# Kernel tuning notes

Hardware: AMD Instinct MI355X
Metric: run time of the kernel (lower is better)

## Reference

```python
import jax, jax.numpy as jnp
import numpy as np

DIM_MODEL = 1024
DIM_K = 1024
DIM_V = 1024


def setup_inputs() -> dict:
    key = jax.random.key(0)
    ks = jax.random.split(key, 7)
    B, S = 4, 2048
    scale = 1.0 / np.sqrt(DIM_MODEL)
    return {
        "x": jax.random.normal(ks[0], (B, S, DIM_MODEL), dtype=jnp.float32),
        # weights stored [in, out] (transpose of torch Linear.weight)
        "Wq": jax.random.normal(ks[1], (DIM_MODEL, DIM_K), dtype=jnp.float32) * scale,
        "Wk": jax.random.normal(ks[2], (DIM_MODEL, DIM_K), dtype=jnp.float32) * scale,
        "Wv": jax.random.normal(ks[3], (DIM_MODEL, DIM_V), dtype=jnp.float32) * scale,
        "Wo": jax.random.normal(ks[4], (DIM_V, DIM_MODEL), dtype=jnp.float32) * (1.0 / np.sqrt(DIM_V)),
        "ln2_gamma": jnp.ones((DIM_MODEL,), dtype=jnp.float32),
        "ln2_beta": jnp.zeros((DIM_MODEL,), dtype=jnp.float32),
    }


def _layernorm(x, gamma, beta, eps=1e-5):
    mu = jnp.mean(x, axis=-1, keepdims=True)
    var = jnp.var(x, axis=-1, keepdims=True)
    return (x - mu) * jax.lax.rsqrt(var + eps) * gamma + beta


def reference(x, Wq, Wk, Wv, Wo, ln2_gamma, ln2_beta):
    # single-head attention, x: [B,S,D]
    q = jnp.einsum("bsd,dk->bsk", x, Wq)
    k = jnp.einsum("bsd,dk->bsk", x, Wk)
    v = jnp.einsum("bsd,dv->bsv", x, Wv)
    scores = jnp.einsum("bqk,bsk->bqs", q, k) / jnp.sqrt(jnp.asarray(DIM_K, x.dtype))
    attn = jax.nn.softmax(scores, axis=-1)  # [B,S,S]
    ctx = jnp.einsum("bqs,bsv->bqv", attn, v)
    hidden = jnp.einsum("bqv,vd->bqd", ctx, Wo)
    hidden = _layernorm(hidden, ln2_gamma, ln2_beta)
    return hidden
```

## Files before the change

kernel.cpp:

```cpp
#include <hip/hip_runtime.h>
#include <hip/hip_bf16.h>
#include <stdint.h>

typedef __bf16 bf16;
typedef __attribute__((ext_vector_type(8))) __bf16 bf16x8;
typedef __attribute__((ext_vector_type(4))) __bf16 bf16x4;
typedef __attribute__((ext_vector_type(4))) float f32x4;

#define AS1 __attribute__((address_space(1)))
#define AS3 __attribute__((address_space(3)))

__device__ __forceinline__ void gl_lds16(const void* g, void* l) {
  __builtin_amdgcn_global_load_lds((const AS1 uint32_t*)g, (AS3 uint32_t*)l, 16, 0, 0);
}

#define FENCE() asm volatile("" ::: "memory")
#define BAR()                        \
  do {                               \
    FENCE();                         \
    __builtin_amdgcn_s_barrier();    \
    FENCE();                         \
  } while (0)
#define VMW4() asm volatile("s_waitcnt vmcnt(4)" ::: "memory")

template <int MODE>
__global__ __launch_bounds__(512, 2) void gemm256(
    const bf16* __restrict__ Abase, const bf16* __restrict__ Bbase,
    bf16* __restrict__ Cbase, int K, int lda, int ldb, int ldc,
    long long sA, long long sB, long long sC, float alpha,
    float* __restrict__ lsum, bf16* __restrict__ C2, bf16* __restrict__ C3) {
  extern __shared__ char smem[];
  const int z = blockIdx.z;
  const bf16* A = Abase + (long long)z * sA;
  const bf16* B = Bbase + (long long)z * sB;
  bf16* C = Cbase + (long long)z * sC;
  const int m0 = blockIdx.y * 256, n0 = blockIdx.x * 256;
  const int t = threadIdx.x;
  const int lane = t & 63;
  const int wid = t >> 6, wrow = wid >> 2, wcol = wid & 3;
  const int quad = lane >> 4, r = lane & 15;

  const int rowq = t >> 3;
  const int chunk = (t & 7) ^ (rowq & 7);
  const bf16* pA0 = A + (long long)(m0 + rowq) * lda + chunk * 8;
  const bf16* pB0 = B + (long long)(n0 + rowq) * ldb + chunk * 8;

  const int aoff = (wrow * 64 + r) * 128;
  const int boff = 32768 + (wcol * 32 + r) * 128;
  const int cs0 = ((quad) ^ (r & 7)) * 16;
  const int cs1 = ((4 + quad) ^ (r & 7)) * 16;

#define STAGE_A(HALF, KT, SB)                                                  \
  do {                                                                         \
    gl_lds16(pA0 + (long long)((HALF) * 128) * lda + (KT),                     \
             (SB) + (HALF) * 16384 + t * 16);                                  \
    gl_lds16(pA0 + (long long)((HALF) * 128 + 64) * lda + (KT),                \
             (SB) + (HALF) * 16384 + 8192 + t * 16);                           \
  } while (0)
#define STAGE_B(HALF, KT, SB)                                                  \
  do {                                                                         \
    gl_lds16(pB0 + (long long)((HALF) * 128) * ldb + (KT),                     \
             (SB) + 32768 + (HALF) * 16384 + t * 16);                          \
    gl_lds16(pB0 + (long long)((HALF) * 128 + 64) * ldb + (KT),                \
             (SB) + 32768 + (HALF) * 16384 + 8192 + t * 16);                   \
  } while (0)
#define READ_A(MH)                                                             \
  _Pragma("unroll") for (int mr = 0; mr < 4; ++mr) {                           \
    af[mr][0] = *(const bf16x8*)(Sc + (MH) * 16384 + aoff + mr * 2048 + cs0);  \
    af[mr][1] = *(const bf16x8*)(Sc + (MH) * 16384 + aoff + mr * 2048 + cs1);  \
  }
#define READ_B(NH)                                                             \
  _Pragma("unroll") for (int nr = 0; nr < 2; ++nr) {                           \
    bfr[NH][nr][0] =                                                           \
        *(const bf16x8*)(Sc + (NH) * 16384 + boff + nr * 2048 + cs0);          \
    bfr[NH][nr][1] =                                                           \
        *(const bf16x8*)(Sc + (NH) * 16384 + boff + nr * 2048 + cs1);          \
  }
#define MMA(MH, NH)                                                            \
  _Pragma("unroll") for (int mr = 0; mr < 4; ++mr)                             \
      _Pragma("unroll") for (int nr = 0; nr < 2; ++nr) {                       \
    acc[MH][NH][mr][nr] = __builtin_amdgcn_mfma_f32_16x16x32_bf16(             \
        af[mr][0], bfr[NH][nr][0], acc[MH][NH][mr][nr], 0, 0, 0);              \
    acc[MH][NH][mr][nr] = __builtin_amdgcn_mfma_f32_16x16x32_bf16(             \
        af[mr][1], bfr[NH][nr][1], acc[MH][NH][mr][nr], 0, 0, 0);              \
  }

  f32x4 acc[2][2][4][2] = {};
  bf16x8 af[4][2];
  bf16x8 bfr[2][2][2];
  char* Sc = smem;
  char* Sn = smem + 65536;
  const int T = K >> 6;

  STAGE_A(0, 0, Sc);
  STAGE_B(0, 0, Sc);
  STAGE_A(1, 0, Sc);
  STAGE_B(1, 0, Sc);
  {
    const int kt1p = (T > 1) ? 64 : 0;
    STAGE_A(0, kt1p, Sn);
    STAGE_B(0, kt1p, Sn);
  }
  VMW4();
  BAR();

  for (int tt = 0; tt < T; ++tt) {
    const int kt1 = (tt + 1 < T ? tt + 1 : 0) << 6;
    const int kt2 = (tt + 2 < T ? tt + 2 : 0) << 6;
    READ_A(0);
    READ_B(0);
    STAGE_A(1, kt1, Sn);
    __builtin_amdgcn_s_setprio(1);
    MMA(0, 0);
    __builtin_amdgcn_s_setprio(0);
    BAR();
    READ_B(1);
    STAGE_B(1, kt1, Sn);
    __builtin_amdgcn_s_setprio(1);
    MMA(0, 1);
    __builtin_amdgcn_s_setprio(0);
    BAR();
    READ_A(1);
    STAGE_A(0, kt2, Sc);
    __builtin_amdgcn_s_setprio(1);
    MMA(1, 0);
    __builtin_amdgcn_s_setprio(0);
    BAR();
    STAGE_B(0, kt2, Sc);
    __builtin_amdgcn_s_setprio(1);
    MMA(1, 1);
    __builtin_amdgcn_s_setprio(0);
    VMW4();
    BAR();
    char* tp = Sc;
    Sc = Sn;
    Sn = tp;
  }

#pragma unroll
  for (int mh = 0; mh < 2; ++mh)
#pragma unroll
    for (int mr = 0; mr < 4; ++mr) {
      const int row0 = m0 + mh * 128 + wrow * 64 + mr * 16 + quad * 4;
      float rsum[4] = {0.f, 0.f, 0.f, 0.f};
#pragma unroll
      for (int nh = 0; nh < 2; ++nh)
#pragma unroll
        for (int nr = 0; nr < 2; ++nr) {
          const int col = n0 + nh * 128 + wcol * 32 + nr * 16 + r;
#pragma unroll
          for (int rg = 0; rg < 4; ++rg) {
            float v = acc[mh][nh][mr][nr][rg] * alpha;
            if constexpr (MODE == 1) {
              bf16 eb = (bf16)__expf(v);
              C[(long long)(row0 + rg) * ldc + col] = eb;
              rsum[rg] += (float)eb;
            } else {
              C[(long long)(row0 + rg) * ldc + col] = (bf16)v;
            }
          }
        }
      if constexpr (MODE == 1) {
#pragma unroll
        for (int rg = 0; rg < 4; ++rg) {
#pragma unroll
          for (int off = 8; off >= 1; off >>= 1)
            rsum[rg] += __shfl_xor(rsum[rg], off);
          if (r == 0)
            atomicAdd(&lsum[(long long)z * 2048 + row0 + rg], rsum[rg]);
        }
      }
    }
#undef STAGE_A
#undef STAGE_B
#undef READ_A
#undef READ_B
#undef MMA
}

template <int MODE>
__global__ __launch_bounds__(256, 3) void gemm128(
    const bf16* __restrict__ Abase, const bf16* __restrict__ Bbase,
    bf16* __restrict__ Cbase, int K, int lda, int ldb, int ldc,
    long long sA, long long sB, long long sC, float alpha,
    float* __restrict__ lsum, bf16* __restrict__ C2, bf16* __restrict__ C3,
    const bf16* __restrict__ A2) {
  extern __shared__ char smem[];
  const int z = blockIdx.z;
  const int bx = blockIdx.x, by = blockIdx.y;
  const bf16* A;
  const bf16* B;
  int m0, n0;
  bool urole = false;
  if constexpr (MODE == 4) {
    if (bx >= 16) {
      urole = true;
      A = A2;
      B = Abase;
      m0 = (bx - 16) * 128;
      n0 = by * 128;
    } else {
      A = Abase;
      B = Bbase;
      m0 = by * 128;
      n0 = bx * 128;
    }
  } else {
    A = Abase + (long long)z * sA;
    B = Bbase + (long long)z * sB;
    m0 = by * 128;
    n0 = bx * 128;
  }
  bf16* C = Cbase + (long long)z * sC;
  const int t = threadIdx.x;
  const int lane = t & 63, wave = t >> 6;
  const int wm = (wave >> 1) * 64, wn = (wave & 1) * 64;
  const int quad = lane >> 4, r = lane & 15;

  const int srow = t >> 3;
  const int schunk = (t & 7) ^ (srow & 7);
  const bf16* ga = A + (long long)(m0 + srow) * lda + schunk * 8;
  const bf16* gb = B + (long long)(n0 + srow) * ldb + schunk * 8;
  if constexpr (MODE == 5) {
    ga += (long long)z * K;
    gb += (long long)z * K;
  }
  char* la = smem + t * 16;
  char* lb = smem + 16384 + t * 16;

  f32x4 acc[4][4] = {};

  for (int k0 = 0; k0 < K; k0 += 64) {
    __syncthreads();
#pragma unroll
    for (int rd = 0; rd < 4; rd++) {
      gl_lds16(ga + (long long)(32 * rd) * lda, la + rd * 4096);
      gl_lds16(gb + (long long)(32 * rd) * ldb, lb + rd * 4096);
    }
    ga += 64;
    gb += 64;
    __syncthreads();

#pragma unroll
    for (int kk = 0; kk < 2; kk++) {
      bf16x8 af[4], bfr[4];
      const int csa = ((kk * 4 + quad) ^ (r & 7)) * 16;
      const char* pa = smem + (wm + r) * 128 + csa;
      const char* pb = smem + 16384 + (wn + r) * 128 + csa;
#pragma unroll
      for (int i = 0; i < 4; i++) af[i] = *(const bf16x8*)(pa + i * 2048);
#pragma unroll
      for (int j = 0; j < 4; j++) bfr[j] = *(const bf16x8*)(pb + j * 2048);
#pragma unroll
      for (int i = 0; i < 4; i++)
#pragma unroll
        for (int j = 0; j < 4; j++)
          acc[i][j] = __builtin_amdgcn_mfma_f32_16x16x32_bf16(af[i], bfr[j],
                                                              acc[i][j], 0, 0, 0);
    }
  }

  if constexpr (MODE == 5) {
    float* Cf = ((float*)Cbase) + (long long)z * 1024 * 1024;
#pragma unroll
    for (int i = 0; i < 4; i++) {
      const int row0 = m0 + wm + i * 16 + quad * 4;
#pragma unroll
      for (int j = 0; j < 4; j++) {
        const int col = n0 + wn + j * 16 + r;
#pragma unroll
        for (int rg = 0; rg < 4; rg++)
          Cf[(long long)(row0 + rg) * 1024 + col] = acc[i][j][rg];
      }
    }
    return;
  }
  if constexpr (MODE == 4) {
    if (urole) {
#pragma unroll
      for (int i = 0; i < 4; i++) {
        const int row0 = m0 + wm + i * 16 + quad * 4;
#pragma unroll
        for (int j = 0; j < 4; j++) {
          const int col = n0 + wn + j * 16 + r;
#pragma unroll
          for (int rg = 0; rg < 4; rg++)
            C3[(long long)(row0 + rg) * 8256 + col] = (bf16)acc[i][j][rg];
        }
      }
      return;
    }
    bf16* dst;
    int c0;
    if (n0 < 1024) {
      dst = Cbase; c0 = n0;
    } else {
      dst = C2; c0 = n0 - 1024;
    }
#pragma unroll
    for (int i = 0; i < 4; i++) {
      const int row0 = m0 + wm + i * 16 + quad * 4;
#pragma unroll
      for (int j = 0; j < 4; j++) {
        const int col = c0 + wn + j * 16 + r;
#pragma unroll
        for (int rg = 0; rg < 4; rg++)
          dst[(long long)(row0 + rg) * 1024 + col] = (bf16)acc[i][j][rg];
      }
    }
    return;
  }

#pragma unroll
  for (int i = 0; i < 4; i++) {
    const int row0 = m0 + wm + i * 16 + quad * 4;
    float inv[4];
    if constexpr (MODE == 2) {
#pragma unroll
      for (int rg = 0; rg < 4; rg++)
        inv[rg] = 1.f / lsum[(long long)z * 2048 + row0 + rg];
    }
#pragma unroll
    for (int j = 0; j < 4; j++) {
      const int col = n0 + wn + j * 16 + r;
#pragma unroll
      for (int rg = 0; rg < 4; rg++) {
        float v = acc[i][j][rg] * alpha;
        if constexpr (MODE == 2) {
          C[(long long)(row0 + rg) * ldc + col] = (bf16)(v * inv[rg]);
        } else {
          C[(long long)(row0 + rg) * ldc + col] = (bf16)v;
        }
      }
    }
  }
}

__global__ __launch_bounds__(256) void prep(
    const float* __restrict__ x, const float* __restrict__ Wq,
    const float* __restrict__ Wk, const float* __restrict__ Wv,
    const float* __restrict__ Wo, bf16* __restrict__ Xb,
    bf16* __restrict__ Wcat, bf16* __restrict__ Wot,
    bf16* __restrict__ Wvb, float* __restrict__ lsum) {
  __shared__ float tile[32][33];
  const int bx = blockIdx.x;
  const int t = threadIdx.x;
  if (bx < 4096) {
    if (bx < 32) lsum[bx * 256 + t] = 0.f;
    long long i = (long long)bx * 256 + t;
    const float4* p = (const float4*)x;
    float4 a = p[i * 2], b = p[i * 2 + 1];
    bf16x8 o;
    o[0] = (bf16)a.x; o[1] = (bf16)a.y; o[2] = (bf16)a.z; o[3] = (bf16)a.w;
    o[4] = (bf16)b.x; o[5] = (bf16)b.y; o[6] = (bf16)b.z; o[7] = (bf16)b.w;
    ((bf16x8*)Xb)[i] = o;
  } else {
    int idx = bx - 4096;
    const int zw = idx >> 10;
    idx &= 1023;
    if (zw == 2) {
      const long long base = (long long)idx * 1024 + t * 4;
      float4 v = *(const float4*)&Wv[base];
      bf16x4 o;
      o[0] = (bf16)v.x; o[1] = (bf16)v.y; o[2] = (bf16)v.z; o[3] = (bf16)v.w;
      *(bf16x4*)&Wvb[base] = o;
      return;
    }
    const int tiy = idx >> 5, tix = idx & 31;
    const float* W = (zw == 0) ? Wq : (zw == 1) ? Wk : Wo;
    bf16* dst = (zw == 0) ? Wcat : (zw == 1) ? (Wcat + 1024 * 1024) : Wot;
    const int bx0 = tix * 32, by0 = tiy * 32;
    const int ttx = t & 31, tty = t >> 5;
#pragma unroll
    for (int i = 0; i < 32; i += 8)
      tile[tty + i][ttx] = W[(long long)(by0 + tty + i) * 1024 + bx0 + ttx];
    __syncthreads();
#pragma unroll
    for (int i = 0; i < 32; i += 8)
      dst[(long long)(bx0 + tty + i) * 1024 + by0 + ttx] = (bf16)tile[ttx][tty + i];
  }
}

__global__ __launch_bounds__(256) void wvo_convert(
    const float* __restrict__ Ff, bf16* __restrict__ Wvo) {
  const long long i8 = ((long long)blockIdx.x * 256 + threadIdx.x) * 8;
  bf16x8 o;
#pragma unroll
  for (int j = 0; j < 8; j++) {
    float s = Ff[i8 + j] + Ff[1048576 + i8 + j] + Ff[2097152 + i8 + j] +
              Ff[3145728 + i8 + j];
    o[j] = (bf16)s;
  }
  *(bf16x8*)&Wvo[i8] = o;
}

__global__ __launch_bounds__(256) void layernorm_rows(
    const bf16* __restrict__ H, const float* __restrict__ gamma,
    const float* __restrict__ beta, float* __restrict__ O) {
  const long long row = blockIdx.x;
  const bf16* h = H + row * 1024;
  float* o = O + row * 1024;
  const int t = threadIdx.x;
  const int lane = t & 63, wave = t >> 6;
  bf16x4 hv = ((const bf16x4*)h)[t];
  float v[4] = {(float)hv[0], (float)hv[1], (float)hv[2], (float)hv[3]};
  float s = v[0] + v[1] + v[2] + v[3];
  float ss = v[0] * v[0] + v[1] * v[1] + v[2] * v[2] + v[3] * v[3];
#pragma unroll
  for (int off = 32; off >= 1; off >>= 1) {
    s += __shfl_xor(s, off);
    ss += __shfl_xor(ss, off);
  }
  __shared__ float rs[4], rss[4];
  if (lane == 0) {
    rs[wave] = s;
    rss[wave] = ss;
  }
  __syncthreads();
  s = rs[0] + rs[1] + rs[2] + rs[3];
  ss = rss[0] + rss[1] + rss[2] + rss[3];
  const float mean = s * (1.f / 1024.f);
  const float var = ss * (1.f / 1024.f) - mean * mean;
  const float rstd = rsqrtf(var + 1e-5f);
  float4 g = ((const float4*)gamma)[t];
  float4 bb = ((const float4*)beta)[t];
  float4 rr;
  rr.x = (v[0] - mean) * rstd * g.x + bb.x;
  rr.y = (v[1] - mean) * rstd * g.y + bb.y;
  rr.z = (v[2] - mean) * rstd * g.z + bb.z;
  rr.w = (v[3] - mean) * rstd * g.w + bb.w;
  ((float4*)o)[t] = rr;
}

extern "C" void kernel_launch(void* const* d_in, const int* in_sizes, int n_in,
                              void* d_out, int out_size, void* d_ws,
                              size_t ws_size, hipStream_t stream) {
  const float* x = (const float*)d_in[0];
  const float* Wq = (const float*)d_in[1];
  const float* Wk = (const float*)d_in[2];
  const float* Wv = (const float*)d_in[3];
  const float* Wo = (const float*)d_in[4];
  const float* gamma = (const float*)d_in[5];
  const float* beta = (const float*)d_in[6];
  float* out = (float*)d_out;

  char* ws = (char*)d_ws;
  const size_t MB = 1024ull * 1024ull;
  bf16* Xb = (bf16*)(ws + 0);
  bf16* Wcat = (bf16*)(ws + 16 * MB);
  bf16* Wot = (bf16*)(ws + 20 * MB);
  bf16* Wvb = (bf16*)(ws + 22 * MB);
  bf16* Qd = (bf16*)(ws + 24 * MB);
  float* Ff = (float*)(ws + 24 * MB);
  bf16* Kd = (bf16*)(ws + 40 * MB);
  bf16* Ut = (bf16*)(ws + 56 * MB);
  bf16* expS = (bf16*)(ws + 73 * MB);
  float* lsum = (float*)(ws + 105 * MB);
  bf16* Wvo = (bf16*)(ws + 106 * MB);
  bf16* Hd = (bf16*)(ws + 108 * MB);

  static int inited = 0;
  if (!inited) {
    hipFuncSetAttribute(reinterpret_cast<const void*>(&gemm256<1>),
                        hipFuncAttributeMaxDynamicSharedMemorySize, 131072);
    inited = 1;
  }

  prep<<<8192, 256, 0, stream>>>(x, Wq, Wk, Wv, Wo, Xb, Wcat, Wot, Wvb, lsum);

  gemm128<5><<<dim3(8, 8, 4), 256, 32768, stream>>>(
      Wot, Wvb, (bf16*)Ff, 256, 1024, 1024, 0, 0, 0, 0, 1.f, nullptr, nullptr,
      nullptr, nullptr);

  wvo_convert<<<512, 256, 0, stream>>>(Ff, Wvo);

  gemm128<4><<<dim3(24, 64, 1), 256, 32768, stream>>>(
      Xb, Wcat, Qd, 1024, 1024, 1024, 1024, 0, 0, 0, 1.f, nullptr, Kd, Ut, Wvo);

  gemm256<1><<<dim3(8, 8, 4), 512, 131072, stream>>>(
      Qd, Kd, expS, 1024, 1024, 1024, 2048, 2048 * 1024LL, 2048 * 1024LL,
      2048 * 2048LL, 0.03125f, lsum, nullptr, nullptr);

  gemm128<2><<<dim3(8, 16, 4), 256, 32768, stream>>>(
      expS, Ut, Hd, 2048, 2048, 8256, 1024, 2048 * 2048LL, 2048LL,
      2048 * 1024LL, 1.f, lsum, nullptr, nullptr, nullptr);

  layernorm_rows<<<8192, 256, 0, stream>>>(Hd, gamma, beta, out);
}
```

Measured before the change: 262.8 us.

## Fold Wo·Wv weight-product GEMM into prep kernel, removing split-K and convert launches

The Wo^T·Wv^T folding GEMM now runs inside the prep kernel as 64 extra blocks. These blocks read the fp32 weights directly, convert them to bf16 on the fly into LDS and run the full K=1024 reduction in one block, writing bf16 Wvo. This removes two kernel launches, the bf16 weight copies and the fp32 split-K partial buffer. The cost is that 64 blocks each do a serial 1024-deep K loop with strided, uncoalesced Wo reads and no async loads, so they may become the tail of the prep kernel.

```diff
diff --git a/kernel.cpp b/kernel.cpp
--- a/kernel.cpp
+++ b/kernel.cpp
@@ -221,10 +221,6 @@
   const int schunk = (t & 7) ^ (srow & 7);
   const bf16* ga = A + (long long)(m0 + srow) * lda + schunk * 8;
   const bf16* gb = B + (long long)(n0 + srow) * ldb + schunk * 8;
-  if constexpr (MODE == 5) {
-    ga += (long long)z * K;
-    gb += (long long)z * K;
-  }
   char* la = smem + t * 16;
   char* lb = smem + 16384 + t * 16;
 
@@ -260,21 +256,6 @@
     }
   }
 
-  if constexpr (MODE == 5) {
-    float* Cf = ((float*)Cbase) + (long long)z * 1024 * 1024;
-#pragma unroll
-    for (int i = 0; i < 4; i++) {
-      const int row0 = m0 + wm + i * 16 + quad * 4;
-#pragma unroll
-      for (int j = 0; j < 4; j++) {
-        const int col = n0 + wn + j * 16 + r;
-#pragma unroll
-        for (int rg = 0; rg < 4; rg++)
-          Cf[(long long)(row0 + rg) * 1024 + col] = acc[i][j][rg];
-      }
-    }
-    return;
-  }
   if constexpr (MODE == 4) {
     if (urole) {
 #pragma unroll
@@ -336,18 +317,87 @@
   }
 }
 
-__global__ __launch_bounds__(256) void prep(
+__global__ __launch_bounds__(256) void prepfold(
     const float* __restrict__ x, const float* __restrict__ Wq,
     const float* __restrict__ Wk, const float* __restrict__ Wv,
     const float* __restrict__ Wo, bf16* __restrict__ Xb,
-    bf16* __restrict__ Wcat, bf16* __restrict__ Wot,
-    bf16* __restrict__ Wvb, float* __restrict__ lsum) {
-  __shared__ float tile[32][33];
+    bf16* __restrict__ Wcat, bf16* __restrict__ Wvo,
+    float* __restrict__ lsum) {
+  __shared__ __align__(16) char sm[32768];
   const int bx = blockIdx.x;
   const int t = threadIdx.x;
-  if (bx < 4096) {
-    if (bx < 32) lsum[bx * 256 + t] = 0.f;
-    long long i = (long long)bx * 256 + t;
+  if (bx < 64) {
+    const int m0 = (bx >> 3) * 128;
+    const int n0 = (bx & 7) * 128;
+    const int lane = t & 63, wave = t >> 6;
+    const int wm = (wave >> 1) * 64, wn = (wave & 1) * 64;
+    const int quad = lane >> 4, r = lane & 15;
+    const int srow = t >> 3;
+    const int c8 = ((t & 7) ^ (srow & 7)) * 8;
+    char* la = sm;
+    char* lb = sm + 16384;
+    f32x4 acc[4][4] = {};
+
+    for (int v0 = 0; v0 < 1024; v0 += 64) {
+      bf16x8 av[4], bv[4];
+#pragma unroll
+      for (int rd = 0; rd < 4; rd++) {
+        const int arow = m0 + srow + 32 * rd;
+        const int brow = n0 + srow + 32 * rd;
+        const int vb = v0 + c8;
+        bf16x8 a8, b8;
+#pragma unroll
+        for (int j = 0; j < 8; j++)
+          a8[j] = (bf16)Wo[(long long)(vb + j) * 1024 + arow];
+        float4 w0 = *(const float4*)&Wv[(long long)brow * 1024 + vb];
+        float4 w1 = *(const float4*)&Wv[(long long)brow * 1024 + vb + 4];
+        b8[0] = (bf16)w0.x; b8[1] = (bf16)w0.y;
+        b8[2] = (bf16)w0.z; b8[3] = (bf16)w0.w;
+        b8[4] = (bf16)w1.x; b8[5] = (bf16)w1.y;
+        b8[6] = (bf16)w1.z; b8[7] = (bf16)w1.w;
+        av[rd] = a8;
+        bv[rd] = b8;
+      }
+      __syncthreads();
+#pragma unroll
+      for (int rd = 0; rd < 4; rd++) {
+        *(bf16x8*)(la + rd * 4096 + t * 16) = av[rd];
+        *(bf16x8*)(lb + rd * 4096 + t * 16) = bv[rd];
+      }
+      __syncthreads();
+#pragma unroll
+      for (int kk = 0; kk < 2; kk++) {
+        bf16x8 af[4], bfr[4];
+        const int csa = ((kk * 4 + quad) ^ (r & 7)) * 16;
+        const char* pa = sm + (wm + r) * 128 + csa;
+        const char* pb = sm + 16384 + (wn + r) * 128 + csa;
+#pragma unroll
+        for (int i = 0; i < 4; i++) af[i] = *(const bf16x8*)(pa + i * 2048);
+#pragma unroll
+        for (int j = 0; j < 4; j++) bfr[j] = *(const bf16x8*)(pb + j * 2048);
+#pragma unroll
+        for (int i = 0; i < 4; i++)
+#pragma unroll
+          for (int j = 0; j < 4; j++)
+            acc[i][j] = __builtin_amdgcn_mfma_f32_16x16x32_bf16(
+                af[i], bfr[j], acc[i][j], 0, 0, 0);
+      }
+    }
+#pragma unroll
+    for (int i = 0; i < 4; i++) {
+      const int row0 = m0 + wm + i * 16 + quad * 4;
+#pragma unroll
+      for (int j = 0; j < 4; j++) {
+        const int col = n0 + wn + j * 16 + r;
+#pragma unroll
+        for (int rg = 0; rg < 4; rg++)
+          Wvo[(long long)(row0 + rg) * 1024 + col] = (bf16)acc[i][j][rg];
+      }
+    }
+  } else if (bx < 4160) {
+    const int i0 = bx - 64;
+    if (i0 < 32) lsum[i0 * 256 + t] = 0.f;
+    long long i = (long long)i0 * 256 + t;
     const float4* p = (const float4*)x;
     float4 a = p[i * 2], b = p[i * 2 + 1];
     bf16x8 o;
@@ -355,20 +405,13 @@
     o[4] = (bf16)b.x; o[5] = (bf16)b.y; o[6] = (bf16)b.z; o[7] = (bf16)b.w;
     ((bf16x8*)Xb)[i] = o;
   } else {
-    int idx = bx - 4096;
+    float (*tile)[33] = (float(*)[33])sm;
+    int idx = bx - 4160;
     const int zw = idx >> 10;
     idx &= 1023;
-    if (zw == 2) {
-      const long long base = (long long)idx * 1024 + t * 4;
-      float4 v = *(const float4*)&Wv[base];
-      bf16x4 o;
-      o[0] = (bf16)v.x; o[1] = (bf16)v.y; o[2] = (bf16)v.z; o[3] = (bf16)v.w;
-      *(bf16x4*)&Wvb[base] = o;
-      return;
-    }
     const int tiy = idx >> 5, tix = idx & 31;
-    const float* W = (zw == 0) ? Wq : (zw == 1) ? Wk : Wo;
-    bf16* dst = (zw == 0) ? Wcat : (zw == 1) ? (Wcat + 1024 * 1024) : Wot;
+    const float* W = (zw == 0) ? Wq : Wk;
+    bf16* dst = Wcat + (long long)zw * 1024 * 1024;
     const int bx0 = tix * 32, by0 = tiy * 32;
     const int ttx = t & 31, tty = t >> 5;
 #pragma unroll
@@ -379,19 +422,6 @@
     for (int i = 0; i < 32; i += 8)
       dst[(long long)(bx0 + tty + i) * 1024 + by0 + ttx] = (bf16)tile[ttx][tty + i];
   }
-}
-
-__global__ __launch_bounds__(256) void wvo_convert(
-    const float* __restrict__ Ff, bf16* __restrict__ Wvo) {
-  const long long i8 = ((long long)blockIdx.x * 256 + threadIdx.x) * 8;
-  bf16x8 o;
-#pragma unroll
-  for (int j = 0; j < 8; j++) {
-    float s = Ff[i8 + j] + Ff[1048576 + i8 + j] + Ff[2097152 + i8 + j] +
-              Ff[3145728 + i8 + j];
-    o[j] = (bf16)s;
-  }
-  *(bf16x8*)&Wvo[i8] = o;
 }
 
 __global__ __launch_bounds__(256) void layernorm_rows(
@@ -448,15 +478,12 @@
   const size_t MB = 1024ull * 1024ull;
   bf16* Xb = (bf16*)(ws + 0);
   bf16* Wcat = (bf16*)(ws + 16 * MB);
-  bf16* Wot = (bf16*)(ws + 20 * MB);
-  bf16* Wvb = (bf16*)(ws + 22 * MB);
+  bf16* Wvo = (bf16*)(ws + 20 * MB);
   bf16* Qd = (bf16*)(ws + 24 * MB);
-  float* Ff = (float*)(ws + 24 * MB);
   bf16* Kd = (bf16*)(ws + 40 * MB);
   bf16* Ut = (bf16*)(ws + 56 * MB);
   bf16* expS = (bf16*)(ws + 73 * MB);
   float* lsum = (float*)(ws + 105 * MB);
-  bf16* Wvo = (bf16*)(ws + 106 * MB);
   bf16* Hd = (bf16*)(ws + 108 * MB);
 
   static int inited = 0;
@@ -466,13 +493,7 @@
     inited = 1;
   }
 
-  prep<<<8192, 256, 0, stream>>>(x, Wq, Wk, Wv, Wo, Xb, Wcat, Wot, Wvb, lsum);
-
-  gemm128<5><<<dim3(8, 8, 4), 256, 32768, stream>>>(
-      Wot, Wvb, (bf16*)Ff, 256, 1024, 1024, 0, 0, 0, 0, 1.f, nullptr, nullptr,
-      nullptr, nullptr);
-
-  wvo_convert<<<512, 256, 0, stream>>>(Ff, Wvo);
+  prepfold<<<6208, 256, 0, stream>>>(x, Wq, Wk, Wv, Wo, Xb, Wcat, Wvo, lsum);
 
   gemm128<4><<<dim3(24, 64, 1), 256, 32768, stream>>>(
       Xb, Wcat, Qd, 1024, 1024, 1024, 1024, 0, 0, 0, 1.f, nullptr, Kd, Ut, Wvo);
```

After: 308.6 us. 17.4% more time.
